# Performance work log

Hardware: AMD Instinct MI355X
Metric: run time of the kernel (lower is better)

Reference implementation:

```python
import jax, jax.numpy as jnp
import numpy as np

NUM_HEADS = 16
ROPE_SEGMENTS = (1024, 512)  # remainder of the sequence is left un-roped
ROPE_THETA = 10000.0
EPS = 1e-6


def _rmsnorm(t, w):
    # t: [B,H,N,D]; norm over last dim in fp32, then scale
    tf = t.astype(jnp.float32)
    n = tf * jax.lax.rsqrt(jnp.mean(tf * tf, axis=-1, keepdims=True) + EPS)
    return n.astype(t.dtype) * w


def _rope(t):
    # t: [B,H,S,D]; positions restart at 0 for each call (segment-local RoPE)
    S, D = t.shape[-2], t.shape[-1]
    inv_freq = 1.0 / (ROPE_THETA ** (jnp.arange(0, D, 2, dtype=jnp.float32) / D))  # [D/2]
    ang = jnp.arange(S, dtype=jnp.float32)[:, None] * inv_freq[None, :]            # [S,D/2]
    cos, sin = jnp.cos(ang), jnp.sin(ang)
    t1, t2 = t[..., : D // 2], t[..., D // 2 :]
    return jnp.concatenate([t1 * cos - t2 * sin, t2 * cos + t1 * sin], axis=-1).astype(t.dtype)


def _segmented_rope(t, N):
    parts, start = [], 0
    for seg in ROPE_SEGMENTS:
        parts.append(_rope(t[:, :, start : start + seg, :]))
        start += seg
    if start < N:
        parts.append(t[:, :, start:, :])
    return jnp.concatenate(parts, axis=2)


def setup_inputs() -> dict:
    key = jax.random.key(0)
    ks = jax.random.split(key, 5)
    B, N, C = 2, 2048, 1024
    D = C // NUM_HEADS
    s = 1.0 / np.sqrt(C)
    return {
        "x": jax.random.normal(ks[0], (B, N, C), jnp.float32),
        "qkv_w": jax.random.normal(ks[1], (3 * C, C), jnp.float32) * s,
        "qkv_b": jax.random.normal(ks[2], (3 * C,), jnp.float32) * 0.02,
        "qn_w": jnp.ones((D,), jnp.float32),
        "kn_w": jnp.ones((D,), jnp.float32),
        "proj_w": jax.random.normal(ks[3], (C, C), jnp.float32) * s,
        "proj_b": jax.random.normal(ks[4], (C,), jnp.float32) * 0.02,
    }


def reference(x, qkv_w, qkv_b, qn_w, kn_w, proj_w, proj_b):
    B, N, C = x.shape
    H = NUM_HEADS
    D = C // H
    qkv = (x @ qkv_w.T + qkv_b).reshape(B, N, 3, H, D)
    qkv = jnp.transpose(qkv, (2, 0, 3, 1, 4))  # [3,B,H,N,D]
    q, k, v = qkv[0], qkv[1], qkv[2]
    q = _rmsnorm(q, qn_w)
    k = _rmsnorm(k, kn_w)
    q = _segmented_rope(q, N)
    k = _segmented_rope(k, N)
    scale = 1.0 / np.sqrt(D)  # SDPA default scale
    scores = jnp.einsum("bhqd,bhkd->bhqk", q, k) * scale
    attn = jax.nn.softmax(scores, axis=-1)
    out = jnp.einsum("bhqk,bhkd->bhqd", attn, v)           # [B,H,N,D]
    out = jnp.transpose(out, (0, 2, 1, 3)).reshape(B, N, C)
    return out @ proj_w.T + proj_b
```

## Files before the change

kernel.cpp:

```cpp
#include <hip/hip_runtime.h>

typedef __attribute__((ext_vector_type(8))) short short8;
typedef __attribute__((ext_vector_type(4))) float f32x4;
typedef __attribute__((ext_vector_type(16))) float f32x16;

__device__ __forceinline__ float bf2f(unsigned short u) {
    union { unsigned int i; float f; } c; c.i = ((unsigned int)u) << 16; return c.f;
}
__device__ __forceinline__ unsigned short f2bf(float f) {
    union { float f; unsigned int i; } c; c.f = f;
    unsigned int u = c.i;
    return (unsigned short)((u + 0x7fffu + ((u >> 16) & 1u)) >> 16);
}

__device__ __forceinline__ void glds16(const void* g, void* l) {
    __builtin_amdgcn_global_load_lds(
        (const __attribute__((address_space(1))) unsigned int*)g,
        (__attribute__((address_space(3))) unsigned int*)l, 16, 0, 0);
}

union i4s8 { int4 i; short8 s; };

#define SCL_F 0.18033688011112042f

__global__ __launch_bounds__(256) void prep(
    const float* __restrict__ x, const float* __restrict__ qkv_w,
    const float* __restrict__ proj_w,
    unsigned short* __restrict__ xb, unsigned short* __restrict__ qwb,
    unsigned short* __restrict__ pwb)
{
    const int b = blockIdx.x, tid = threadIdx.x;
    const float* src; unsigned short* dst; int i;
    if (b < 4096)      { src = x;      dst = xb;  i = b * 256 + tid; }
    else if (b < 7168) { src = qkv_w;  dst = qwb; i = (b - 4096) * 256 + tid; }
    else               { src = proj_w; dst = pwb; i = (b - 7168) * 256 + tid; }
    float4 v = ((const float4*)src)[i];
    ushort4 o;
    o.x = f2bf(v.x); o.y = f2bf(v.y); o.z = f2bf(v.z); o.w = f2bf(v.w);
    ((ushort4*)dst)[i] = o;
}

__global__ __launch_bounds__(256) void gemm_qkv(
    const unsigned short* __restrict__ A,
    const unsigned short* __restrict__ W,
    const float* __restrict__ bias,
    const float* __restrict__ qn_w, const float* __restrict__ kn_w,
    unsigned short* __restrict__ qb, unsigned short* __restrict__ kb,
    unsigned short* __restrict__ vt)
{
    __shared__ unsigned short pool[128 * 136];
    const int tid = threadIdx.x;
    const int w = tid >> 6, l = tid & 63, quad = l >> 4, low = l & 15;
    const int m0 = blockIdx.y * 128, n0 = blockIdx.x * 128;
    const int wm = w >> 1, wn = w & 1;
    const int K = 1024;

    f32x4 acc[4][4];
#pragma unroll
    for (int i = 0; i < 4; i++)
#pragma unroll
        for (int j = 0; j < 4; j++) acc[i][j] = (f32x4){0.f, 0.f, 0.f, 0.f};

    const int r1 = tid >> 3, p1 = tid & 7, c1 = p1 ^ (r1 & 7);
    const unsigned short* ga = A + (size_t)(m0 + r1) * K + c1 * 8;
    const unsigned short* gw = W + (size_t)(n0 + r1) * K + c1 * 8;
    char* lA = (char*)pool + (w << 10);
    char* lW = (char*)pool + 16384 + (w << 10);

    for (int k0 = 0; k0 < K; k0 += 64) {
        __syncthreads();
        glds16(ga + k0,            lA);
        glds16(ga + k0 + 32 * K,   lA + 4096);
        glds16(ga + k0 + 64 * K,   lA + 8192);
        glds16(ga + k0 + 96 * K,   lA + 12288);
        glds16(gw + k0,            lW);
        glds16(gw + k0 + 32 * K,   lW + 4096);
        glds16(gw + k0 + 64 * K,   lW + 8192);
        glds16(gw + k0 + 96 * K,   lW + 12288);
        __syncthreads();
#pragma unroll
        for (int ks = 0; ks < 2; ks++) {
            short8 af[4], wf[4];
#pragma unroll
            for (int i = 0; i < 4; i++) {
                const int ra = wm * 64 + i * 16 + low;
                af[i] = *(const short8*)&pool[ra * 64 + ((ks * 4 + quad) ^ (ra & 7)) * 8];
                const int rw = wn * 64 + i * 16 + low;
                wf[i] = *(const short8*)&pool[8192 + rw * 64 + ((ks * 4 + quad) ^ (rw & 7)) * 8];
            }
#pragma unroll
            for (int i = 0; i < 4; i++)
#pragma unroll
                for (int j = 0; j < 4; j++)
                    acc[i][j] = __builtin_amdgcn_mfma_f32_16x16x32_bf16(
                        af[i], wf[j], acc[i][j], 0, 0, 0);
        }
    }

    const int colbase = n0 + wn * 64;
    const int t3 = n0 >> 10;
    const int hh = (colbase & 1023) >> 6;

    if (t3 == 2) {
        __syncthreads();
#pragma unroll
        for (int i = 0; i < 4; i++)
#pragma unroll
            for (int j = 0; j < 4; j++) {
                const int c = wn * 64 + j * 16 + low;
                const float bv = bias[n0 + c];
#pragma unroll
                for (int reg = 0; reg < 4; reg++) {
                    const int r = wm * 64 + i * 16 + quad * 4 + reg;
                    pool[c * 136 + r] = f2bf(acc[i][j][reg] + bv);
                }
            }
        __syncthreads();
        const int b_ = m0 >> 11, nbase = m0 & 2047;
        const int rch = (tid & 15) * 8;
#pragma unroll
        for (int p = 0; p < 8; p++) {
            const int c = (tid >> 4) + p * 16;
            const int gc = n0 + c;
            const int h2 = (gc & 1023) >> 6, d = gc & 63;
            const short8 vv = *(const short8*)&pool[c * 136 + rch];
            *(short8*)(vt + ((size_t)((b_ * 16 + h2) * 64 + d)) * 2048 + nbase + rch) = vv;
        }
        return;
    }

    const float* nw = (t3 == 0) ? qn_w : kn_w;
    const float wscl = (t3 == 0) ? SCL_F : 1.0f;
    float wv4[4];
#pragma unroll
    for (int j = 0; j < 4; j++) wv4[j] = nw[j * 16 + low] * wscl;
    const float c0 = -2.0f * 13.287712379549449f / 64.0f;
    const float invA = exp2f(c0 * (float)low);
    const float invB = exp2f(c0 * (float)(16 + low));
    unsigned short* dqk = (t3 == 0) ? qb : kb;

#pragma unroll
    for (int i = 0; i < 4; i++) {
#pragma unroll
        for (int reg = 0; reg < 4; reg++) {
            const int gm = m0 + wm * 64 + i * 16 + quad * 4 + reg;
            const int b_ = gm >> 11, npos = gm & 2047;
            float v[4];
#pragma unroll
            for (int j = 0; j < 4; j++)
                v[j] = acc[i][j][reg] + bias[colbase + j * 16 + low];
            float ss = v[0]*v[0] + v[1]*v[1] + v[2]*v[2] + v[3]*v[3];
            ss += __shfl_xor(ss, 1); ss += __shfl_xor(ss, 2);
            ss += __shfl_xor(ss, 4); ss += __shfl_xor(ss, 8);
            const float r = rsqrtf(ss * (1.0f / 64.0f) + 1e-6f);
            float nv[4];
#pragma unroll
            for (int j = 0; j < 4; j++) nv[j] = v[j] * r * wv4[j];
            float o0, o1, o2, o3;
            if (npos < 1536) {
                const float p = (float)((npos < 1024) ? npos : (npos - 1024));
                float sA, cA, sB, cB;
                __sincosf(p * invA, &sA, &cA);
                __sincosf(p * invB, &sB, &cB);
                o0 = nv[0] * cA - nv[2] * sA;
                o1 = nv[1] * cB - nv[3] * sB;
                o2 = nv[2] * cA + nv[0] * sA;
                o3 = nv[3] * cB + nv[1] * sB;
            } else { o0 = nv[0]; o1 = nv[1]; o2 = nv[2]; o3 = nv[3]; }
            unsigned short* drow =
                dqk + ((size_t)(b_ * 16 + hh) * 2048 + npos) * 64 + low;
            drow[0]  = f2bf(o0);
            drow[16] = f2bf(o1);
            drow[32] = f2bf(o2);
            drow[48] = f2bf(o3);
        }
    }
}

__global__ __launch_bounds__(256, 4) void flash_mfma(
    const unsigned short* __restrict__ qg, const unsigned short* __restrict__ kg,
    const unsigned short* __restrict__ vg, unsigned short* __restrict__ po,
    float* __restrict__ pl)
{
    __shared__ unsigned short Ks[128 * 64];
    __shared__ unsigned short Vs[64 * 128];

    const int tid = threadIdx.x;
    const int w = tid >> 6, lane = tid & 63, h5 = lane >> 5, l5 = lane & 31;
    const int bh = blockIdx.y, q0 = blockIdx.x * 128, half = blockIdx.z;

    short8 qf[4];
    {
        const unsigned short* qrow = qg + ((size_t)bh * 2048 + q0 + w * 32 + l5) * 64;
#pragma unroll
        for (int ks = 0; ks < 4; ks++)
            qf[ks] = *(const short8*)(qrow + ks * 16 + h5 * 8);
    }

    f32x16 o0, o1, ls;
#pragma unroll
    for (int i = 0; i < 16; i++) { o0[i] = 0.f; o1[i] = 0.f; ls[i] = 0.f; }
    i4s8 ones; ones.i = make_int4(0x3F803F80, 0x3F803F80, 0x3F803F80, 0x3F803F80);

    const int krr = tid >> 3, kc = (tid & 7) ^ (krr & 7);
    const unsigned short* gk = kg + ((size_t)bh * 2048 + krr) * 64 + kc * 8;
    const int vrr = tid >> 4, vc = (tid & 15) ^ (vrr & 15);
    const unsigned short* gv = vg + ((size_t)bh * 64 + vrr) * 2048 + vc * 8;
    char* lK = (char*)Ks + (w << 10);
    char* lV = (char*)Vs + (w << 10);
    const int kbase = half * 1024;

    for (int kt = 0; kt < 8; kt++) {
        const size_t ko = (size_t)(kbase + kt * 128);
        __syncthreads();
        glds16(gk + ko * 64,         lK);
        glds16(gk + ko * 64 + 2048,  lK + 4096);
        glds16(gk + ko * 64 + 4096,  lK + 8192);
        glds16(gk + ko * 64 + 6144,  lK + 12288);
        glds16(gv + ko,              lV);
        glds16(gv + ko + 32768,      lV + 4096);
        glds16(gv + ko + 65536,      lV + 8192);
        glds16(gv + ko + 98304,      lV + 12288);
        __syncthreads();

#pragma unroll
        for (int kbk = 0; kbk < 4; kbk++) {
            f32x16 s;
#pragma unroll
            for (int i = 0; i < 16; i++) s[i] = 0.f;
            const int krow = kbk * 32 + l5;
#pragma unroll
            for (int ks = 0; ks < 4; ks++) {
                const int ch = (h5 + 2 * ks) ^ (krow & 7);
                const short8 kf = *(const short8*)&Ks[krow * 64 + ch * 8];
                s = __builtin_amdgcn_mfma_f32_32x32x16_bf16(kf, qf[ks], s, 0, 0, 0);
            }
            unsigned int dw[8], pdw[8];
#pragma unroll
            for (int r = 0; r < 8; r++) {
                union { float f; unsigned int u; } a, b;
                a.f = exp2f(s[2 * r]);
                b.f = exp2f(s[2 * r + 1]);
                dw[r] = __builtin_amdgcn_perm(b.u, a.u, 0x07060302u);
            }
#pragma unroll
            for (int r = 0; r < 8; r++) pdw[r] = __shfl_xor((int)dw[r], 32);
            i4s8 f0, f1;
            f0.i.x = h5 ? pdw[2] : dw[0];
            f0.i.y = h5 ? pdw[3] : dw[1];
            f0.i.z = h5 ? dw[2]  : pdw[0];
            f0.i.w = h5 ? dw[3]  : pdw[1];
            f1.i.x = h5 ? pdw[6] : dw[4];
            f1.i.y = h5 ? pdw[7] : dw[5];
            f1.i.z = h5 ? dw[6]  : pdw[4];
            f1.i.w = h5 ? dw[7]  : pdw[5];

            ls = __builtin_amdgcn_mfma_f32_32x32x16_bf16(f0.s, ones.s, ls, 0, 0, 0);
            ls = __builtin_amdgcn_mfma_f32_32x32x16_bf16(f1.s, ones.s, ls, 0, 0, 0);

#pragma unroll
            for (int nb = 0; nb < 2; nb++) {
                const int vrow = nb * 32 + l5;
                const int chb = kbk * 4 + h5;
                const short8 vfa = *(const short8*)&Vs[vrow * 128 + ((chb    ) ^ (vrow & 15)) * 8];
                const short8 vfb = *(const short8*)&Vs[vrow * 128 + ((chb + 2) ^ (vrow & 15)) * 8];
                f32x16& oo = nb ? o1 : o0;
                oo = __builtin_amdgcn_mfma_f32_32x32x16_bf16(f0.s, vfa, oo, 0, 0, 0);
                oo = __builtin_amdgcn_mfma_f32_32x32x16_bf16(f1.s, vfb, oo, 0, 0, 0);
            }
        }
    }

    unsigned short* pob = po + ((size_t)(half * 32 + bh)) * 2048 * 64;
    float* plb = pl + ((size_t)(half * 32 + bh)) * 2048;
#pragma unroll
    for (int r = 0; r < 16; r++) {
        const int qrow = q0 + w * 32 + (r & 3) + 8 * (r >> 2) + 4 * h5;
        pob[(size_t)qrow * 64 + l5]      = f2bf(o0[r]);
        pob[(size_t)qrow * 64 + 32 + l5] = f2bf(o1[r]);
        if (l5 == 0) plb[qrow] = ls[r];
    }
}

__global__ __launch_bounds__(256) void combine(
    const unsigned short* __restrict__ po, const float* __restrict__ pl,
    unsigned short* __restrict__ ao)
{
    const int g = blockIdx.x * 256 + threadIdx.x;
    const int row = g >> 3;
    const int c8 = (g & 7) * 8;
    const int bh = row >> 11, n = row & 2047;
    const float inv = 1.0f / (pl[row] + pl[65536 + row]);
    const short8 a = *(const short8*)(po + (size_t)row * 64 + c8);
    const short8 b = *(const short8*)(po + 4194304 + (size_t)row * 64 + c8);
    short8 r;
#pragma unroll
    for (int j = 0; j < 8; j++)
        r[j] = (short)f2bf((bf2f((unsigned short)a[j]) + bf2f((unsigned short)b[j])) * inv);
    const int b_ = bh >> 4, h = bh & 15;
    *(short8*)(ao + ((size_t)(b_ * 2048 + n)) * 1024 + h * 64 + c8) = r;
}

__global__ __launch_bounds__(256) void gemm_out(
    const unsigned short* __restrict__ A,
    const unsigned short* __restrict__ W,
    const float* __restrict__ bias,
    float* __restrict__ outp)
{
    __shared__ unsigned short As[64 * 64];
    __shared__ unsigned short Ws[128 * 64];
    const int tid = threadIdx.x;
    const int w = tid >> 6, l = tid & 63, quad = l >> 4, low = l & 15;
    const int m0 = blockIdx.y * 64, n0 = blockIdx.x * 128;
    const int wm = w >> 1, wn = w & 1;
    const int K = 1024;

    f32x4 acc[2][4];
#pragma unroll
    for (int i = 0; i < 2; i++)
#pragma unroll
        for (int j = 0; j < 4; j++) acc[i][j] = (f32x4){0.f, 0.f, 0.f, 0.f};

    const int r1 = tid >> 3, p1 = tid & 7, c1 = p1 ^ (r1 & 7);
    const unsigned short* ga = A + (size_t)(m0 + r1) * K + c1 * 8;
    const unsigned short* gw = W + (size_t)(n0 + r1) * K + c1 * 8;
    char* lA = (char*)As + (w << 10);
    char* lW = (char*)Ws + (w << 10);

    for (int k0 = 0; k0 < K; k0 += 64) {
        __syncthreads();
        glds16(ga + k0,           lA);
        glds16(ga + k0 + 32 * K,  lA + 4096);
        glds16(gw + k0,           lW);
        glds16(gw + k0 + 32 * K,  lW + 4096);
        glds16(gw + k0 + 64 * K,  lW + 8192);
        glds16(gw + k0 + 96 * K,  lW + 12288);
        __syncthreads();
#pragma unroll
        for (int ks = 0; ks < 2; ks++) {
            short8 af[2], wf[4];
#pragma unroll
            for (int i = 0; i < 2; i++) {
                const int ra = wm * 32 + i * 16 + low;
                af[i] = *(const short8*)&As[ra * 64 + ((ks * 4 + quad) ^ (ra & 7)) * 8];
            }
#pragma unroll
            for (int j = 0; j < 4; j++) {
                const int rw = wn * 64 + j * 16 + low;
                wf[j] = *(const short8*)&Ws[rw * 64 + ((ks * 4 + quad) ^ (rw & 7)) * 8];
            }
#pragma unroll
            for (int i = 0; i < 2; i++)
#pragma unroll
                for (int j = 0; j < 4; j++)
                    acc[i][j] = __builtin_amdgcn_mfma_f32_16x16x32_bf16(
                        af[i], wf[j], acc[i][j], 0, 0, 0);
        }
    }

#pragma unroll
    for (int i = 0; i < 2; i++)
#pragma unroll
        for (int j = 0; j < 4; j++) {
            const int gc = n0 + wn * 64 + j * 16 + low;
            const float bv = bias[gc];
#pragma unroll
            for (int reg = 0; reg < 4; reg++) {
                const int gm = m0 + wm * 32 + i * 16 + quad * 4 + reg;
                outp[(size_t)gm * 1024 + gc] = acc[i][j][reg] + bv;
            }
        }
}

extern "C" void kernel_launch(void* const* d_in, const int* in_sizes, int n_in,
                              void* d_out, int out_size, void* d_ws, size_t ws_size,
                              hipStream_t stream)
{
    const float* x      = (const float*)d_in[0];
    const float* qkv_w  = (const float*)d_in[1];
    const float* qkv_b  = (const float*)d_in[2];
    const float* qn_w   = (const float*)d_in[3];
    const float* kn_w   = (const float*)d_in[4];
    const float* proj_w = (const float*)d_in[5];
    const float* proj_b = (const float*)d_in[6];

    char* base = (char*)d_ws;
    unsigned short* pwb = (unsigned short*)(base + 256);
    unsigned short* qb  = pwb + 1048576;
    unsigned short* kb  = qb  + 4194304;
    unsigned short* vt  = kb  + 4194304;
    unsigned short* ao  = vt  + 4194304;
    unsigned short* xb  = ao  + 4194304;
    unsigned short* qwb = xb  + 4194304;
    unsigned short* po  = xb;
    float* pl           = (float*)(po + 8388608);

    prep<<<8192, 256, 0, stream>>>(x, qkv_w, proj_w, xb, qwb, pwb);

    gemm_qkv<<<dim3(24, 32), 256, 0, stream>>>(xb, qwb, qkv_b, qn_w, kn_w,
                                               qb, kb, vt);

    flash_mfma<<<dim3(16, 32, 2), 256, 0, stream>>>(qb, kb, vt, po, pl);

    combine<<<2048, 256, 0, stream>>>(po, pl, ao);

    gemm_out<<<dim3(8, 64), 256, 0, stream>>>(ao, pwb, proj_b, (float*)d_out);
}
```

Baseline: 205.3 us.

## Retile output GEMM with 32x32 MFMA, grid-stride prep, remap flash block order

```diff
diff --git a/kernel.cpp b/kernel.cpp
--- a/kernel.cpp
+++ b/kernel.cpp
@@ -29,15 +29,18 @@
     unsigned short* __restrict__ xb, unsigned short* __restrict__ qwb,
     unsigned short* __restrict__ pwb)
 {
-    const int b = blockIdx.x, tid = threadIdx.x;
-    const float* src; unsigned short* dst; int i;
-    if (b < 4096)      { src = x;      dst = xb;  i = b * 256 + tid; }
-    else if (b < 7168) { src = qkv_w;  dst = qwb; i = (b - 4096) * 256 + tid; }
-    else               { src = proj_w; dst = pwb; i = (b - 7168) * 256 + tid; }
-    float4 v = ((const float4*)src)[i];
-    ushort4 o;
-    o.x = f2bf(v.x); o.y = f2bf(v.y); o.z = f2bf(v.z); o.w = f2bf(v.w);
-    ((ushort4*)dst)[i] = o;
+    const int TX = 1048576, TQ = 786432, TP = 262144;
+    const int total = TX + TQ + TP;
+    for (int i = blockIdx.x * 256 + threadIdx.x; i < total; i += 2048 * 256) {
+        const float* src; unsigned short* dst; int j;
+        if (i < TX)           { src = x;      dst = xb;  j = i; }
+        else if (i < TX + TQ) { src = qkv_w;  dst = qwb; j = i - TX; }
+        else                  { src = proj_w; dst = pwb; j = i - TX - TQ; }
+        float4 v = ((const float4*)src)[j];
+        ushort4 o;
+        o.x = f2bf(v.x); o.y = f2bf(v.y); o.z = f2bf(v.z); o.w = f2bf(v.w);
+        ((ushort4*)dst)[j] = o;
+    }
 }
 
 __global__ __launch_bounds__(256) void gemm_qkv(
@@ -187,7 +190,10 @@
 
     const int tid = threadIdx.x;
     const int w = tid >> 6, lane = tid & 63, h5 = lane >> 5, l5 = lane & 31;
-    const int bh = blockIdx.y, q0 = blockIdx.x * 128, half = blockIdx.z;
+    const int id = blockIdx.x;
+    const int bh = id & 31;
+    const int q0 = ((id >> 5) & 15) * 128;
+    const int half = id >> 9;
 
     short8 qf[4];
     {
@@ -301,75 +307,59 @@
     *(short8*)(ao + ((size_t)(b_ * 2048 + n)) * 1024 + h * 64 + c8) = r;
 }
 
-__global__ __launch_bounds__(256) void gemm_out(
+__global__ __launch_bounds__(128) void gemm_out(
     const unsigned short* __restrict__ A,
     const unsigned short* __restrict__ W,
     const float* __restrict__ bias,
     float* __restrict__ outp)
 {
-    __shared__ unsigned short As[64 * 64];
-    __shared__ unsigned short Ws[128 * 64];
+    __shared__ unsigned short pool[8192];
     const int tid = threadIdx.x;
-    const int w = tid >> 6, l = tid & 63, quad = l >> 4, low = l & 15;
-    const int m0 = blockIdx.y * 64, n0 = blockIdx.x * 128;
-    const int wm = w >> 1, wn = w & 1;
+    const int w = tid >> 6, lane = tid & 63, h5 = lane >> 5, l5 = lane & 31;
+    const int m0 = blockIdx.y * 64, n0 = blockIdx.x * 64;
     const int K = 1024;
 
-    f32x4 acc[2][4];
-#pragma unroll
-    for (int i = 0; i < 2; i++)
-#pragma unroll
-        for (int j = 0; j < 4; j++) acc[i][j] = (f32x4){0.f, 0.f, 0.f, 0.f};
-
-    const int r1 = tid >> 3, p1 = tid & 7, c1 = p1 ^ (r1 & 7);
-    const unsigned short* ga = A + (size_t)(m0 + r1) * K + c1 * 8;
-    const unsigned short* gw = W + (size_t)(n0 + r1) * K + c1 * 8;
-    char* lA = (char*)As + (w << 10);
-    char* lW = (char*)Ws + (w << 10);
+    f32x16 acc0, acc1;
+#pragma unroll
+    for (int i = 0; i < 16; i++) { acc0[i] = 0.f; acc1[i] = 0.f; }
+
+    const int rr = tid >> 3, cc = (tid & 7) ^ (rr & 7);
+    const unsigned short* ga = A + (size_t)(m0 + rr) * K + cc * 8;
+    const unsigned short* gw = W + (size_t)(n0 + rr) * K + cc * 8;
+    char* lA = (char*)pool + (w << 10);
+    char* lW = (char*)pool + 8192 + (w << 10);
 
     for (int k0 = 0; k0 < K; k0 += 64) {
         __syncthreads();
         glds16(ga + k0,           lA);
+        glds16(ga + k0 + 16 * K,  lA + 2048);
         glds16(ga + k0 + 32 * K,  lA + 4096);
+        glds16(ga + k0 + 48 * K,  lA + 6144);
         glds16(gw + k0,           lW);
+        glds16(gw + k0 + 16 * K,  lW + 2048);
         glds16(gw + k0 + 32 * K,  lW + 4096);
-        glds16(gw + k0 + 64 * K,  lW + 8192);
-        glds16(gw + k0 + 96 * K,  lW + 12288);
-        __syncthreads();
-#pragma unroll
-        for (int ks = 0; ks < 2; ks++) {
-            short8 af[2], wf[4];
-#pragma unroll
-            for (int i = 0; i < 2; i++) {
-                const int ra = wm * 32 + i * 16 + low;
-                af[i] = *(const short8*)&As[ra * 64 + ((ks * 4 + quad) ^ (ra & 7)) * 8];
-            }
-#pragma unroll
-            for (int j = 0; j < 4; j++) {
-                const int rw = wn * 64 + j * 16 + low;
-                wf[j] = *(const short8*)&Ws[rw * 64 + ((ks * 4 + quad) ^ (rw & 7)) * 8];
-            }
-#pragma unroll
-            for (int i = 0; i < 2; i++)
-#pragma unroll
-                for (int j = 0; j < 4; j++)
-                    acc[i][j] = __builtin_amdgcn_mfma_f32_16x16x32_bf16(
-                        af[i], wf[j], acc[i][j], 0, 0, 0);
-        }
-    }
-
-#pragma unroll
-    for (int i = 0; i < 2; i++)
-#pragma unroll
-        for (int j = 0; j < 4; j++) {
-            const int gc = n0 + wn * 64 + j * 16 + low;
-            const float bv = bias[gc];
-#pragma unroll
-            for (int reg = 0; reg < 4; reg++) {
-                const int gm = m0 + wm * 32 + i * 16 + quad * 4 + reg;
-                outp[(size_t)gm * 1024 + gc] = acc[i][j][reg] + bv;
-            }
-        }
+        glds16(gw + k0 + 48 * K,  lW + 6144);
+        __syncthreads();
+        const int ra = w * 32 + l5;
+#pragma unroll
+        for (int ks = 0; ks < 4; ks++) {
+            const int ch = (ks << 1) | h5;
+            const short8 af  = *(const short8*)&pool[ra * 64 + (ch ^ (ra & 7)) * 8];
+            const short8 wf0 = *(const short8*)&pool[4096 + l5 * 64 + (ch ^ (l5 & 7)) * 8];
+            const int rw1 = 32 + l5;
+            const short8 wf1 = *(const short8*)&pool[4096 + rw1 * 64 + (ch ^ (rw1 & 7)) * 8];
+            acc0 = __builtin_amdgcn_mfma_f32_32x32x16_bf16(af, wf0, acc0, 0, 0, 0);
+            acc1 = __builtin_amdgcn_mfma_f32_32x32x16_bf16(af, wf1, acc1, 0, 0, 0);
+        }
+    }
+
+    const float b0 = bias[n0 + l5], b1 = bias[n0 + 32 + l5];
+#pragma unroll
+    for (int r = 0; r < 16; r++) {
+        const int gm = m0 + w * 32 + (r & 3) + 8 * (r >> 2) + 4 * h5;
+        outp[(size_t)gm * 1024 + n0 + l5]      = acc0[r] + b0;
+        outp[(size_t)gm * 1024 + n0 + 32 + l5] = acc1[r] + b1;
+    }
 }
 
 extern "C" void kernel_launch(void* const* d_in, const int* in_sizes, int n_in,
@@ -395,14 +385,14 @@
     unsigned short* po  = xb;
     float* pl           = (float*)(po + 8388608);
 
-    prep<<<8192, 256, 0, stream>>>(x, qkv_w, proj_w, xb, qwb, pwb);
+    prep<<<2048, 256, 0, stream>>>(x, qkv_w, proj_w, xb, qwb, pwb);
 
     gemm_qkv<<<dim3(24, 32), 256, 0, stream>>>(xb, qwb, qkv_b, qn_w, kn_w,
                                                qb, kb, vt);
 
-    flash_mfma<<<dim3(16, 32, 2), 256, 0, stream>>>(qb, kb, vt, po, pl);
+    flash_mfma<<<1024, 256, 0, stream>>>(qb, kb, vt, po, pl);
 
     combine<<<2048, 256, 0, stream>>>(po, pl, ao);
 
-    gemm_out<<<dim3(8, 64), 256, 0, stream>>>(ao, pwb, proj_b, (float*)d_out);
-}
+    gemm_out<<<dim3(16, 64), 128, 0, stream>>>(ao, pwb, proj_b, (float*)d_out);
+}
```

Result: no change. 206.6 us (+0.6%).
